# Performance work log

Hardware: AMD Instinct MI355X
Metric: run time of the kernel (lower is better)

The kernel has to match this reference:

```python
import jax, jax.numpy as jnp
import numpy as np

LOW_THRESH = 0.3   # below -> background (label 0)
HIGH_THRESH = 0.7  # at/above -> foreground (label 1); in-between -> ignore (-1)


def _make_boxes(key, n):
    # two random corners per box -> valid (y1,x1,y2,x2) via min/max
    c = jax.random.uniform(key, (n, 2, 2), dtype=jnp.float32)
    lo = jnp.min(c, axis=1)
    hi = jnp.max(c, axis=1)
    return jnp.concatenate([lo, hi], axis=-1)  # [n, 4] = (y1, x1, y2, x2)


def setup_inputs() -> dict:
    key = jax.random.key(0)
    k1, k2 = jax.random.split(key)
    boxes1 = _make_boxes(k1, 262144)  # anchors / proposals
    boxes2 = _make_boxes(k2, 128)     # ground-truth boxes
    return {"boxes1": boxes1, "boxes2": boxes2}


def pairwise_iou(boxes1, boxes2):
    # boxes: (y1, x1, y2, x2). Result: [N1, N2]
    area1 = (boxes1[:, 2] - boxes1[:, 0]) * (boxes1[:, 3] - boxes1[:, 1])  # [N1]
    area2 = (boxes2[:, 2] - boxes2[:, 0]) * (boxes2[:, 3] - boxes2[:, 1])  # [N2]
    # intersection corners, broadcast [N1,1] vs [N2]
    iy1 = jnp.maximum(boxes1[:, None, 0], boxes2[None, :, 0])
    ix1 = jnp.maximum(boxes1[:, None, 1], boxes2[None, :, 1])
    iy2 = jnp.minimum(boxes1[:, None, 2], boxes2[None, :, 2])
    ix2 = jnp.minimum(boxes1[:, None, 3], boxes2[None, :, 3])
    inter = jnp.maximum(iy2 - iy1, 0.0) * jnp.maximum(ix2 - ix1, 0.0)  # [N1, N2]
    union = area1[:, None] + area2[None, :] - inter
    return inter / jnp.maximum(union, 1e-10)


def reference(boxes1, boxes2):
    iou = pairwise_iou(boxes1, boxes2)          # [N1, N2]
    matched_vals = jnp.max(iou, axis=1)         # [N1] best IoU per anchor
    matched_idx = jnp.argmax(iou, axis=1)       # [N1] index of best gt box
    labels = jnp.where(
        matched_vals >= HIGH_THRESH,
        jnp.int32(1),
        jnp.where(matched_vals < LOW_THRESH, jnp.int32(0), jnp.int32(-1)),
    )
    return matched_vals, matched_idx, labels
```

## Files before the change

kernel.cpp:

```cpp
#include <hip/hip_runtime.h>

#define N2 128
#define BLOCK 256
#define APB 64

__global__ __launch_bounds__(BLOCK, 8) void matcher_kernel(
    const float4* __restrict__ boxes1,
    const float4* __restrict__ boxes2,
    float* __restrict__ out_vals,
    float* __restrict__ out_idx,
    float* __restrict__ out_labels,
    int n1)
{
#pragma clang fp contract(off)
    __shared__ float s_area2[N2];
    __shared__ float s_q[4][APB];
    __shared__ int   s_ix[4][APB];

    const int t = threadIdx.x;
    if (t < N2) {
        const float4 b = boxes2[t];
        s_area2[t] = (b.z - b.x) * (b.w - b.y);
    }
    __syncthreads();

    const int w    = __builtin_amdgcn_readfirstlane(t >> 6);
    const int lane = t & 63;
    const int i    = blockIdx.x * APB + lane;
    const bool valid = (i < n1);

    const float4 a = boxes1[valid ? i : 0];
    const float area1 = (a.z - a.x) * (a.w - a.y);

    float best = -1.0f;
    int   bidx = 0;

    const int j0 = w * 32;
#pragma unroll 8
    for (int k = 0; k < 32; ++k) {
        const int j = j0 + k;
        const float4 b = boxes2[j];
        const float a2 = s_area2[j];
        const float iy1 = fmaxf(a.x, b.x);
        const float ix1 = fmaxf(a.y, b.y);
        const float iy2 = fminf(a.z, b.z);
        const float ix2 = fminf(a.w, b.w);
        const float hy = fmaxf(iy2 - iy1, 0.0f);
        const float hx = fmaxf(ix2 - ix1, 0.0f);
        const float inter = hy * hx;
        const float uni = (area1 + a2) - inter;
        const float q = inter / fmaxf(uni, 1e-10f);
        if (q > best) { best = q; bidx = j; }
    }

    s_q[w][lane]  = best;
    s_ix[w][lane] = bidx;
    __syncthreads();

    if (t < APB) {
        const int ii = blockIdx.x * APB + t;
        if (ii < n1) {
            float q  = s_q[0][t];
            int   ix = s_ix[0][t];
#pragma unroll
            for (int w2 = 1; w2 < 4; ++w2) {
                const float q2 = s_q[w2][t];
                if (q2 > q) { q = q2; ix = s_ix[w2][t]; }
            }
            out_vals[ii]   = q;
            out_idx[ii]    = (float)ix;
            out_labels[ii] = (q >= 0.7f) ? 1.0f : ((q < 0.3f) ? 0.0f : -1.0f);
        }
    }
}

extern "C" void kernel_launch(void* const* d_in, const int* in_sizes, int n_in,
                              void* d_out, int out_size, void* d_ws, size_t ws_size,
                              hipStream_t stream) {
    const float4* boxes1 = (const float4*)d_in[0];
    const float4* boxes2 = (const float4*)d_in[1];
    const int n1 = in_sizes[0] / 4;

    float* out = (float*)d_out;
    float* out_vals   = out;
    float* out_idx    = out + n1;
    float* out_labels = out + 2 * n1;

    const int grid = (n1 + APB - 1) / APB;
    matcher_kernel<<<grid, BLOCK, 0, stream>>>(boxes1, boxes2,
                                               out_vals, out_idx, out_labels, n1);
}
```

Baseline: 29.02 us.

## Use approximate reciprocal with exact fallback, stage boxes2 in LDS, two anchors per thread

```diff
diff --git a/kernel.cpp b/kernel.cpp
--- a/kernel.cpp
+++ b/kernel.cpp
@@ -2,7 +2,8 @@
 
 #define N2 128
 #define BLOCK 256
-#define APB 64
+#define APB 128
+#define BAND 9.5367431640625e-07f
 
 __global__ __launch_bounds__(BLOCK, 8) void matcher_kernel(
     const float4* __restrict__ boxes1,
@@ -13,48 +14,101 @@
     int n1)
 {
 #pragma clang fp contract(off)
-    __shared__ float s_area2[N2];
-    __shared__ float s_q[4][APB];
-    __shared__ int   s_ix[4][APB];
+    __shared__ float4 s_b2[N2];
+    __shared__ float  s_area2[N2];
+    __shared__ float  s_q[4][APB];
+    __shared__ int    s_ix[4][APB];
 
     const int t = threadIdx.x;
     if (t < N2) {
         const float4 b = boxes2[t];
+        s_b2[t] = b;
         s_area2[t] = (b.z - b.x) * (b.w - b.y);
     }
     __syncthreads();
 
     const int w    = __builtin_amdgcn_readfirstlane(t >> 6);
     const int lane = t & 63;
-    const int i    = blockIdx.x * APB + lane;
-    const bool valid = (i < n1);
+    const int i0   = blockIdx.x * APB + lane;
+    const int i1   = i0 + 64;
 
-    const float4 a = boxes1[valid ? i : 0];
-    const float area1 = (a.z - a.x) * (a.w - a.y);
-
-    float best = -1.0f;
-    int   bidx = 0;
+    const float4 a0 = boxes1[(i0 < n1) ? i0 : 0];
+    const float4 a1 = boxes1[(i1 < n1) ? i1 : 0];
+    const float ar0 = (a0.z - a0.x) * (a0.w - a0.y);
+    const float ar1 = (a1.z - a1.x) * (a1.w - a1.y);
 
     const int j0 = w * 32;
-#pragma unroll 8
+    float bq0 = -1.0f, bq1 = -1.0f;
+    int   bx0 = j0,    bx1 = j0;
+    bool  slow = false;
+
+#pragma unroll 2
     for (int k = 0; k < 32; ++k) {
         const int j = j0 + k;
-        const float4 b = boxes2[j];
+        const float4 b = s_b2[j];
         const float a2 = s_area2[j];
-        const float iy1 = fmaxf(a.x, b.x);
-        const float ix1 = fmaxf(a.y, b.y);
-        const float iy2 = fminf(a.z, b.z);
-        const float ix2 = fminf(a.w, b.w);
-        const float hy = fmaxf(iy2 - iy1, 0.0f);
-        const float hx = fmaxf(ix2 - ix1, 0.0f);
-        const float inter = hy * hx;
-        const float uni = (area1 + a2) - inter;
-        const float q = inter / fmaxf(uni, 1e-10f);
-        if (q > best) { best = q; bidx = j; }
+        {
+            const float hy = fmaxf(fminf(a0.z, b.z) - fmaxf(a0.x, b.x), 0.0f);
+            const float hx = fmaxf(fminf(a0.w, b.w) - fmaxf(a0.y, b.y), 0.0f);
+            const float inter = hy * hx;
+            const float um = fmaxf((ar0 + a2) - inter, 1e-10f);
+            const float q = inter * __builtin_amdgcn_rcpf(um);
+            const float d = q - bq0;
+            const float th = bq0 * BAND;
+            slow = slow | ((inter > 0.0f) & (fabsf(d) <= th));
+            if (d > th) { bq0 = q; bx0 = j; }
+        }
+        {
+            const float hy = fmaxf(fminf(a1.z, b.z) - fmaxf(a1.x, b.x), 0.0f);
+            const float hx = fmaxf(fminf(a1.w, b.w) - fmaxf(a1.y, b.y), 0.0f);
+            const float inter = hy * hx;
+            const float um = fmaxf((ar1 + a2) - inter, 1e-10f);
+            const float q = inter * __builtin_amdgcn_rcpf(um);
+            const float d = q - bq1;
+            const float th = bq1 * BAND;
+            slow = slow | ((inter > 0.0f) & (fabsf(d) <= th));
+            if (d > th) { bq1 = q; bx1 = j; }
+        }
     }
 
-    s_q[w][lane]  = best;
-    s_ix[w][lane] = bidx;
+#define FRAC(J, AA, AR, INTER, UM)                                    \
+    {                                                                 \
+        const float4 b = s_b2[(J)];                                   \
+        const float hy = fmaxf(fminf(AA.z, b.z) - fmaxf(AA.x, b.x), 0.0f); \
+        const float hx = fmaxf(fminf(AA.w, b.w) - fmaxf(AA.y, b.y), 0.0f); \
+        INTER = hy * hx;                                              \
+        UM = fmaxf(((AR) + s_area2[(J)]) - INTER, 1e-10f);            \
+    }
+
+    if (slow) {
+        float b0 = -1.0f, b1 = -1.0f;
+        int   x0 = j0,    x1 = j0;
+        for (int k = 0; k < 32; ++k) {
+            const int j = j0 + k;
+            float in0, um0, in1, um1;
+            FRAC(j, a0, ar0, in0, um0)
+            FRAC(j, a1, ar1, in1, um1)
+            const float q0 = in0 / um0;
+            const float q1 = in1 / um1;
+            if (q0 > b0) { b0 = q0; x0 = j; }
+            if (q1 > b1) { b1 = q1; x1 = j; }
+        }
+        bx0 = x0; bx1 = x1;
+    }
+
+    float qe0, qe1;
+    {
+        float in0, um0, in1, um1;
+        FRAC(bx0, a0, ar0, in0, um0)
+        FRAC(bx1, a1, ar1, in1, um1)
+        qe0 = in0 / um0;
+        qe1 = in1 / um1;
+    }
+
+    s_q[w][lane]       = qe0;
+    s_ix[w][lane]      = bx0;
+    s_q[w][lane + 64]  = qe1;
+    s_ix[w][lane + 64] = bx1;
     __syncthreads();
 
     if (t < APB) {
```

Result: slower. 30.97 us (+6.7%).

## Process two anchors per thread with approximate rcp IoU and exact refinement

Applied to the files above, without the earlier changes.

```diff
diff --git a/kernel.cpp b/kernel.cpp
--- a/kernel.cpp
+++ b/kernel.cpp
@@ -2,7 +2,8 @@
 
 #define N2 128
 #define BLOCK 256
-#define APB 64
+#define APB 128
+#define BAND 3.814697265625e-06f
 
 __global__ __launch_bounds__(BLOCK, 8) void matcher_kernel(
     const float4* __restrict__ boxes1,
@@ -26,35 +27,88 @@
 
     const int w    = __builtin_amdgcn_readfirstlane(t >> 6);
     const int lane = t & 63;
-    const int i    = blockIdx.x * APB + lane;
-    const bool valid = (i < n1);
+    const int i0   = blockIdx.x * APB + lane;
+    const int i1   = i0 + 64;
 
-    const float4 a = boxes1[valid ? i : 0];
-    const float area1 = (a.z - a.x) * (a.w - a.y);
-
-    float best = -1.0f;
-    int   bidx = 0;
+    const float4 a0 = boxes1[(i0 < n1) ? i0 : 0];
+    const float4 a1 = boxes1[(i1 < n1) ? i1 : 0];
+    const float ar0 = (a0.z - a0.x) * (a0.w - a0.y);
+    const float ar1 = (a1.z - a1.x) * (a1.w - a1.y);
 
     const int j0 = w * 32;
+    float bq0 = -1.0f, b20 = -1.0f; int bx0 = 0;
+    float bq1 = -1.0f, b21 = -1.0f; int bx1 = 0;
+
 #pragma unroll 8
     for (int k = 0; k < 32; ++k) {
         const int j = j0 + k;
         const float4 b = boxes2[j];
         const float a2 = s_area2[j];
-        const float iy1 = fmaxf(a.x, b.x);
-        const float ix1 = fmaxf(a.y, b.y);
-        const float iy2 = fminf(a.z, b.z);
-        const float ix2 = fminf(a.w, b.w);
-        const float hy = fmaxf(iy2 - iy1, 0.0f);
-        const float hx = fmaxf(ix2 - ix1, 0.0f);
-        const float inter = hy * hx;
-        const float uni = (area1 + a2) - inter;
-        const float q = inter / fmaxf(uni, 1e-10f);
-        if (q > best) { best = q; bidx = j; }
+        {
+            const float hy = fmaxf(fminf(a0.z, b.z) - fmaxf(a0.x, b.x), 0.0f);
+            const float hx = fmaxf(fminf(a0.w, b.w) - fmaxf(a0.y, b.y), 0.0f);
+            const float inter = hy * hx;
+            const float S = ar0 + a2;
+            const float q = fmaxf(inter * __builtin_amdgcn_rcpf(S), 0.0f);
+            b20 = fmaxf(b20, fminf(bq0, q));
+            const bool cc = q > bq0;
+            bq0 = fmaxf(bq0, q);
+            bx0 = cc ? k : bx0;
+        }
+        {
+            const float hy = fmaxf(fminf(a1.z, b.z) - fmaxf(a1.x, b.x), 0.0f);
+            const float hx = fmaxf(fminf(a1.w, b.w) - fmaxf(a1.y, b.y), 0.0f);
+            const float inter = hy * hx;
+            const float S = ar1 + a2;
+            const float q = fmaxf(inter * __builtin_amdgcn_rcpf(S), 0.0f);
+            b21 = fmaxf(b21, fminf(bq1, q));
+            const bool cc = q > bq1;
+            bq1 = fmaxf(bq1, q);
+            bx1 = cc ? k : bx1;
+        }
     }
 
-    s_q[w][lane]  = best;
-    s_ix[w][lane] = bidx;
+    int bidx0 = j0 + bx0;
+    int bidx1 = j0 + bx1;
+    const bool slow0 = (bq0 > 0.0f) && ((bq0 - b20) <= bq0 * BAND);
+    const bool slow1 = (bq1 > 0.0f) && ((bq1 - b21) <= bq1 * BAND);
+
+#define REFQ(AA, AR, J, QOUT)                                             \
+    {                                                                     \
+        const float4 b = boxes2[(J)];                                     \
+        const float wa2 = (b.z - b.x) * (b.w - b.y);                      \
+        const float hy = fmaxf(fminf(AA.z, b.z) - fmaxf(AA.x, b.x), 0.0f);\
+        const float hx = fmaxf(fminf(AA.w, b.w) - fmaxf(AA.y, b.y), 0.0f);\
+        const float inter = hy * hx;                                      \
+        const float um = fmaxf(((AR) + wa2) - inter, 1e-10f);             \
+        QOUT = inter / um;                                                \
+    }
+
+    if (slow0) {
+        float best = -1.0f; int bx = j0;
+        for (int k = 0; k < 32; ++k) {
+            float qq; REFQ(a0, ar0, j0 + k, qq)
+            if (qq > best) { best = qq; bx = j0 + k; }
+        }
+        bidx0 = bx;
+    }
+    if (slow1) {
+        float best = -1.0f; int bx = j0;
+        for (int k = 0; k < 32; ++k) {
+            float qq; REFQ(a1, ar1, j0 + k, qq)
+            if (qq > best) { best = qq; bx = j0 + k; }
+        }
+        bidx1 = bx;
+    }
+
+    float qe0, qe1;
+    REFQ(a0, ar0, bidx0, qe0)
+    REFQ(a1, ar1, bidx1, qe1)
+
+    s_q[w][lane]       = qe0;
+    s_ix[w][lane]      = bidx0;
+    s_q[w][lane + 64]  = qe1;
+    s_ix[w][lane + 64] = bidx1;
     __syncthreads();
 
     if (t < APB) {
```

After: 27.06 us. 6.8% less time.

## Use approximate reciprocal IoU with exact refinement, and give each thread four anchors

Applied to the files above, without the earlier changes.

```diff
diff --git a/kernel.cpp b/kernel.cpp
--- a/kernel.cpp
+++ b/kernel.cpp
@@ -1,8 +1,10 @@
 #include <hip/hip_runtime.h>
 
 #define N2 128
-#define BLOCK 256
-#define APB 64
+#define BLOCK 512
+#define APB 256
+#define WIN 16
+#define BAND 3.814697265625e-06f
 
 __global__ __launch_bounds__(BLOCK, 8) void matcher_kernel(
     const float4* __restrict__ boxes1,
@@ -14,8 +16,8 @@
 {
 #pragma clang fp contract(off)
     __shared__ float s_area2[N2];
-    __shared__ float s_q[4][APB];
-    __shared__ int   s_ix[4][APB];
+    __shared__ float s_q[8][APB];
+    __shared__ int   s_ix[8][APB];
 
     const int t = threadIdx.x;
     if (t < N2) {
@@ -26,44 +28,76 @@
 
     const int w    = __builtin_amdgcn_readfirstlane(t >> 6);
     const int lane = t & 63;
-    const int i    = blockIdx.x * APB + lane;
-    const bool valid = (i < n1);
+    const int base = blockIdx.x * APB;
 
-    const float4 a = boxes1[valid ? i : 0];
-    const float area1 = (a.z - a.x) * (a.w - a.y);
+    float4 A[4]; float AR[4];
+#pragma unroll
+    for (int m = 0; m < 4; ++m) {
+        const int i = base + lane + m * 64;
+        A[m] = boxes1[(i < n1) ? i : 0];
+        AR[m] = (A[m].z - A[m].x) * (A[m].w - A[m].y);
+    }
 
-    float best = -1.0f;
-    int   bidx = 0;
+    const int j0 = w * WIN;
+    float bq[4] = {-1.0f, -1.0f, -1.0f, -1.0f};
+    float b2[4] = {-1.0f, -1.0f, -1.0f, -1.0f};
+    int   bx[4] = {0, 0, 0, 0};
 
-    const int j0 = w * 32;
 #pragma unroll 8
-    for (int k = 0; k < 32; ++k) {
+    for (int k = 0; k < WIN; ++k) {
         const int j = j0 + k;
         const float4 b = boxes2[j];
         const float a2 = s_area2[j];
-        const float iy1 = fmaxf(a.x, b.x);
-        const float ix1 = fmaxf(a.y, b.y);
-        const float iy2 = fminf(a.z, b.z);
-        const float ix2 = fminf(a.w, b.w);
-        const float hy = fmaxf(iy2 - iy1, 0.0f);
-        const float hx = fmaxf(ix2 - ix1, 0.0f);
-        const float inter = hy * hx;
-        const float uni = (area1 + a2) - inter;
-        const float q = inter / fmaxf(uni, 1e-10f);
-        if (q > best) { best = q; bidx = j; }
+#pragma unroll
+        for (int m = 0; m < 4; ++m) {
+            const float hy = fmaxf(fminf(A[m].z, b.z) - fmaxf(A[m].x, b.x), 0.0f);
+            const float hx = fmaxf(fminf(A[m].w, b.w) - fmaxf(A[m].y, b.y), 0.0f);
+            const float inter = hy * hx;
+            const float S = AR[m] + a2;
+            const float q = fmaxf(inter * __builtin_amdgcn_rcpf(S), 0.0f);
+            b2[m] = fmaxf(b2[m], fminf(bq[m], q));
+            const bool cc = q > bq[m];
+            bq[m] = fmaxf(bq[m], q);
+            bx[m] = cc ? k : bx[m];
+        }
     }
 
-    s_q[w][lane]  = best;
-    s_ix[w][lane] = bidx;
+#define REFQ(M, J, QOUT)                                                   \
+    {                                                                      \
+        const float4 b = boxes2[(J)];                                      \
+        const float wa2 = (b.z - b.x) * (b.w - b.y);                       \
+        const float hy = fmaxf(fminf(A[M].z, b.z) - fmaxf(A[M].x, b.x), 0.0f); \
+        const float hx = fmaxf(fminf(A[M].w, b.w) - fmaxf(A[M].y, b.y), 0.0f); \
+        const float inter = hy * hx;                                       \
+        const float um = fmaxf((AR[M] + wa2) - inter, 1e-10f);             \
+        QOUT = inter / um;                                                 \
+    }
+
+#pragma unroll
+    for (int m = 0; m < 4; ++m) {
+        int bidx = j0 + bx[m];
+        const bool slow = (bq[m] > 0.0f) && ((bq[m] - b2[m]) <= bq[m] * BAND);
+        if (slow) {
+            float best = -1.0f; int bxx = j0;
+            for (int k = 0; k < WIN; ++k) {
+                float qq; REFQ(m, j0 + k, qq)
+                if (qq > best) { best = qq; bxx = j0 + k; }
+            }
+            bidx = bxx;
+        }
+        float qe; REFQ(m, bidx, qe)
+        s_q[w][lane + m * 64]  = qe;
+        s_ix[w][lane + m * 64] = bidx;
+    }
     __syncthreads();
 
     if (t < APB) {
-        const int ii = blockIdx.x * APB + t;
+        const int ii = base + t;
         if (ii < n1) {
             float q  = s_q[0][t];
             int   ix = s_ix[0][t];
 #pragma unroll
-            for (int w2 = 1; w2 < 4; ++w2) {
+            for (int w2 = 1; w2 < 8; ++w2) {
                 const float q2 = s_q[w2][t];
                 if (q2 > q) { q = q2; ix = s_ix[w2][t]; }
             }
```

After: 25.72 us. -11.4%, faster.
